# Performance work log

Hardware: AMD Instinct MI355X
Metric: run time of the kernel (lower is better)

The kernel has to match this reference:

```python
import jax, jax.numpy as jnp
import numpy as np

NUM_BINS = 256


def _rgb_to_yuv(rgb):  # [B,3,H,W]
    r, g, b = rgb[:, 0], rgb[:, 1], rgb[:, 2]
    y = 0.299 * r + 0.587 * g + 0.114 * b
    u = -0.147 * r - 0.289 * g + 0.436 * b
    v = 0.615 * r - 0.515 * g - 0.100 * b
    return jnp.stack([y, u, v], axis=1)


def _yuv_to_rgb(yuv):  # [B,3,H,W]
    y, u, v = yuv[:, 0], yuv[:, 1], yuv[:, 2]
    r = y + 1.14 * v
    g = y - 0.396 * u - 0.581 * v
    b = y + 2.029 * u
    return jnp.stack([r, g, b], axis=1)


def _equalize_channel(ch):
    # ch: [H, W] in [0, 1]; replicates kornia/TF equalize on one channel.
    im = ch * 255.0
    flat = im.reshape(-1)
    # histc(bins=256, min=0, max=255): bin width 255/256
    bin_idx = jnp.clip(jnp.floor(flat * (NUM_BINS / 255.0)).astype(jnp.int32), 0, NUM_BINS - 1)
    histo = jax.ops.segment_sum(jnp.ones_like(flat), bin_idx, num_segments=NUM_BINS)
    # last nonzero histogram value
    nz = histo > 0
    last_idx = (NUM_BINS - 1) - jnp.argmax(nz[::-1])
    last_val = histo[last_idx]
    step = jnp.floor((jnp.sum(histo) - last_val) / 255.0)  # integer floor-div semantics
    safe_step = jnp.maximum(step, 1.0)
    lut = jnp.floor((jnp.cumsum(histo) + jnp.floor(step / 2.0)) / safe_step)
    lut = jnp.concatenate([jnp.zeros((1,), lut.dtype), lut[:-1]])
    lut = jnp.clip(lut, 0.0, 255.0)
    gather_idx = jnp.clip(flat.astype(jnp.int32), 0, NUM_BINS - 1)
    mapped = jnp.take(lut, gather_idx)
    out = jnp.where(step == 0.0, flat, mapped)
    return (out / 255.0).reshape(ch.shape)


def setup_inputs() -> dict:
    key = jax.random.key(0)
    img = jax.random.uniform(key, (16, 3, 1024, 1024), dtype=jnp.float32)
    return {"img": img}


def reference(img) -> jnp.ndarray:
    img = jnp.clip(img, 0.0, 1.0)
    yuv = _rgb_to_yuv(img)
    y_eq = jax.vmap(_equalize_channel)(yuv[:, 0])  # [B,H,W]
    yuv = jnp.concatenate([y_eq[:, None], yuv[:, 1:]], axis=1)
    return _yuv_to_rgb(yuv)
```

## Files before the change

kernel.cpp:

```cpp
#include <hip/hip_runtime.h>

#define NPIX   (1024*1024)
#define NBATCH 16
#define NBINS  256

__device__ __forceinline__ float clamp01(float x) {
    return fminf(fmaxf(x, 0.0f), 1.0f);
}

__global__ void __launch_bounds__(256)
hist_kernel(const float* __restrict__ img, unsigned int* __restrict__ hist) {
    const int b = blockIdx.y;
    __shared__ unsigned int lh[NBINS];
    if (threadIdx.x < NBINS) lh[threadIdx.x] = 0u;
    __syncthreads();

    const float* base = img + (size_t)b * 3 * NPIX;
    const float4* r4 = (const float4*)(base);
    const float4* g4 = (const float4*)(base + NPIX);
    const float4* b4 = (const float4*)(base + 2 * NPIX);

    const int n4 = NPIX / 4;
    const int stride = gridDim.x * blockDim.x;
    for (int i = blockIdx.x * blockDim.x + threadIdx.x; i < n4; i += stride) {
        float4 rv = r4[i], gv = g4[i], bv = b4[i];
        float rr[4] = {rv.x, rv.y, rv.z, rv.w};
        float gg[4] = {gv.x, gv.y, gv.z, gv.w};
        float bb[4] = {bv.x, bv.y, bv.z, bv.w};
#pragma unroll
        for (int k = 0; k < 4; ++k) {
            float r = clamp01(rr[k]);
            float g = clamp01(gg[k]);
            float bl = clamp01(bb[k]);
            float y = 0.299f * r + 0.587f * g + 0.114f * bl;
            float flat = y * 255.0f;
            int bin = (int)floorf(flat * (256.0f / 255.0f));
            bin = bin < 0 ? 0 : (bin > NBINS - 1 ? NBINS - 1 : bin);
            atomicAdd(&lh[bin], 1u);
        }
    }
    __syncthreads();
    if (threadIdx.x < NBINS)
        atomicAdd(&hist[b * NBINS + threadIdx.x], lh[threadIdx.x]);
}

__global__ void __launch_bounds__(256)
lut_kernel(const unsigned int* __restrict__ hist,
           float* __restrict__ lut, float* __restrict__ stepflag) {
    const int b = blockIdx.x;
    const int i = threadIdx.x;
    __shared__ float h[NBINS];
    __shared__ float scan[NBINS];
    __shared__ float s_step, s_half;

    h[i] = (float)hist[b * NBINS + i];
    __syncthreads();

    if (i == 0) {
        float total = 0.0f;
        int last = 0;
        for (int k = 0; k < NBINS; ++k) {
            float hv = h[k];
            total += hv;
            if (hv > 0.0f) last = k;
        }
        float step = floorf((total - h[last]) / 255.0f);
        s_step = step;
        s_half = floorf(step / 2.0f);
        float cum = 0.0f;
        for (int k = 0; k < NBINS; ++k) { cum += h[k]; scan[k] = cum; }
        stepflag[b] = step;
    }
    __syncthreads();

    float step = s_step;
    float safe = fmaxf(step, 1.0f);
    float l = (i == 0) ? 0.0f : floorf((scan[i - 1] + s_half) / safe);
    l = fminf(fmaxf(l, 0.0f), 255.0f);
    lut[b * NBINS + i] = l;
}

__global__ void __launch_bounds__(256)
apply_kernel(const float* __restrict__ img, float* __restrict__ out,
             const float* __restrict__ lut, const float* __restrict__ stepflag) {
    const int b = blockIdx.y;
    __shared__ float llut[NBINS];
    if (threadIdx.x < NBINS) llut[threadIdx.x] = lut[b * NBINS + threadIdx.x];
    __syncthreads();

    const float step = stepflag[b];
    const bool identity = (step == 0.0f);

    const float* base  = img + (size_t)b * 3 * NPIX;
    float*       obase = out + (size_t)b * 3 * NPIX;
    const float4* r4 = (const float4*)(base);
    const float4* g4 = (const float4*)(base + NPIX);
    const float4* b4 = (const float4*)(base + 2 * NPIX);
    float4* ro = (float4*)(obase);
    float4* go = (float4*)(obase + NPIX);
    float4* bo = (float4*)(obase + 2 * NPIX);

    const int n4 = NPIX / 4;
    const int stride = gridDim.x * blockDim.x;
    for (int i = blockIdx.x * blockDim.x + threadIdx.x; i < n4; i += stride) {
        float4 rv = r4[i], gv = g4[i], bv = b4[i];
        float rr[4] = {rv.x, rv.y, rv.z, rv.w};
        float gg[4] = {gv.x, gv.y, gv.z, gv.w};
        float bb[4] = {bv.x, bv.y, bv.z, bv.w};
        float orr[4], org[4], orb[4];
#pragma unroll
        for (int k = 0; k < 4; ++k) {
            float r = clamp01(rr[k]);
            float g = clamp01(gg[k]);
            float bl = clamp01(bb[k]);
            float y = 0.299f * r + 0.587f * g + 0.114f * bl;
            float u = -0.147f * r - 0.289f * g + 0.436f * bl;
            float v = 0.615f * r - 0.515f * g - 0.1f * bl;

            float flat = y * 255.0f;
            int gi = (int)flat;
            gi = gi < 0 ? 0 : (gi > NBINS - 1 ? NBINS - 1 : gi);
            float ye = identity ? flat : llut[gi];
            ye = ye / 255.0f;

            orr[k] = ye + 1.14f * v;
            org[k] = ye - 0.396f * u - 0.581f * v;
            orb[k] = ye + 2.029f * u;
        }
        ro[i] = make_float4(orr[0], orr[1], orr[2], orr[3]);
        go[i] = make_float4(org[0], org[1], org[2], org[3]);
        bo[i] = make_float4(orb[0], orb[1], orb[2], orb[3]);
    }
}

extern "C" void kernel_launch(void* const* d_in, const int* in_sizes, int n_in,
                              void* d_out, int out_size, void* d_ws, size_t ws_size,
                              hipStream_t stream) {
    const float* img = (const float*)d_in[0];
    float* out = (float*)d_out;

    unsigned int* hist = (unsigned int*)d_ws;
    float* lut      = (float*)((char*)d_ws + NBATCH * NBINS * 4);
    float* stepflag = (float*)((char*)d_ws + 2 * NBATCH * NBINS * 4);

    hipMemsetAsync(d_ws, 0, NBATCH * NBINS * sizeof(unsigned int), stream);

    const int BPB = 64;
    dim3 grid(BPB, NBATCH), block(256);
    hist_kernel<<<grid, block, 0, stream>>>(img, hist);
    lut_kernel<<<NBATCH, NBINS, 0, stream>>>(hist, lut, stepflag);
    apply_kernel<<<grid, block, 0, stream>>>(img, out, lut, stepflag);
}
```

Measured before the change: 405.6 us.

## Privatize histogram sub-bins, parallelize LUT scan, double grid, nontemporal stores

The histogram kernel now keeps four padded sub-histograms in shared memory, one per thread lane group, to reduce atomic contention on shared-memory bins. The LUT kernel replaces its single-thread serial loops with a parallel prefix scan and a max-reduction for the last nonzero bin. Blocks per batch go from 64 to 128, and the apply kernel uses nontemporal stores and multiplies by a reciprocal instead of dividing. The reciprocal multiply can differ from the reference division by one ulp, and the removed lower clamp relies on the luma value never being negative.

```diff
diff --git a/kernel.cpp b/kernel.cpp
--- a/kernel.cpp
+++ b/kernel.cpp
@@ -3,6 +3,11 @@
 #define NPIX   (1024*1024)
 #define NBATCH 16
 #define NBINS  256
+#define NSUB   4
+#define SUBST  257
+#define BPB    128
+
+typedef float v4f __attribute__((ext_vector_type(4)));
 
 __device__ __forceinline__ float clamp01(float x) {
     return fminf(fmaxf(x, 0.0f), 1.0f);
@@ -11,37 +16,40 @@
 __global__ void __launch_bounds__(256)
 hist_kernel(const float* __restrict__ img, unsigned int* __restrict__ hist) {
     const int b = blockIdx.y;
-    __shared__ unsigned int lh[NBINS];
-    if (threadIdx.x < NBINS) lh[threadIdx.x] = 0u;
+    __shared__ unsigned int lh[NSUB * SUBST];
+    for (int k = threadIdx.x; k < NSUB * SUBST; k += 256) lh[k] = 0u;
     __syncthreads();
 
+    const int sub = (threadIdx.x & (NSUB - 1)) * SUBST;
+
     const float* base = img + (size_t)b * 3 * NPIX;
-    const float4* r4 = (const float4*)(base);
-    const float4* g4 = (const float4*)(base + NPIX);
-    const float4* b4 = (const float4*)(base + 2 * NPIX);
+    const v4f* r4 = (const v4f*)(base);
+    const v4f* g4 = (const v4f*)(base + NPIX);
+    const v4f* b4 = (const v4f*)(base + 2 * NPIX);
 
     const int n4 = NPIX / 4;
     const int stride = gridDim.x * blockDim.x;
     for (int i = blockIdx.x * blockDim.x + threadIdx.x; i < n4; i += stride) {
-        float4 rv = r4[i], gv = g4[i], bv = b4[i];
-        float rr[4] = {rv.x, rv.y, rv.z, rv.w};
-        float gg[4] = {gv.x, gv.y, gv.z, gv.w};
-        float bb[4] = {bv.x, bv.y, bv.z, bv.w};
+        v4f rv = r4[i], gv = g4[i], bv = b4[i];
 #pragma unroll
         for (int k = 0; k < 4; ++k) {
-            float r = clamp01(rr[k]);
-            float g = clamp01(gg[k]);
-            float bl = clamp01(bb[k]);
+            float r = clamp01(rv[k]);
+            float g = clamp01(gv[k]);
+            float bl = clamp01(bv[k]);
             float y = 0.299f * r + 0.587f * g + 0.114f * bl;
             float flat = y * 255.0f;
             int bin = (int)floorf(flat * (256.0f / 255.0f));
             bin = bin < 0 ? 0 : (bin > NBINS - 1 ? NBINS - 1 : bin);
-            atomicAdd(&lh[bin], 1u);
+            atomicAdd(&lh[sub + bin], 1u);
         }
     }
     __syncthreads();
-    if (threadIdx.x < NBINS)
-        atomicAdd(&hist[b * NBINS + threadIdx.x], lh[threadIdx.x]);
+    {
+        const int t = threadIdx.x;
+        unsigned int s = lh[0 * SUBST + t] + lh[1 * SUBST + t] +
+                         lh[2 * SUBST + t] + lh[3 * SUBST + t];
+        atomicAdd(&hist[b * NBINS + t], s);
+    }
 }
 
 __global__ void __launch_bounds__(256)
@@ -49,35 +57,42 @@
            float* __restrict__ lut, float* __restrict__ stepflag) {
     const int b = blockIdx.x;
     const int i = threadIdx.x;
-    __shared__ float h[NBINS];
-    __shared__ float scan[NBINS];
-    __shared__ float s_step, s_half;
+    __shared__ float sc[NBINS];
+    __shared__ int   li[NBINS];
 
-    h[i] = (float)hist[b * NBINS + i];
+    float hv = (float)hist[b * NBINS + i];
+    sc[i] = hv;
+    li[i] = (hv > 0.0f) ? i : -1;
     __syncthreads();
 
-    if (i == 0) {
-        float total = 0.0f;
-        int last = 0;
-        for (int k = 0; k < NBINS; ++k) {
-            float hv = h[k];
-            total += hv;
-            if (hv > 0.0f) last = k;
-        }
-        float step = floorf((total - h[last]) / 255.0f);
-        s_step = step;
-        s_half = floorf(step / 2.0f);
-        float cum = 0.0f;
-        for (int k = 0; k < NBINS; ++k) { cum += h[k]; scan[k] = cum; }
-        stepflag[b] = step;
+#pragma unroll
+    for (int off = 1; off < NBINS; off <<= 1) {
+        float v = (i >= off) ? sc[i - off] : 0.0f;
+        __syncthreads();
+        sc[i] += v;
+        __syncthreads();
     }
-    __syncthreads();
+#pragma unroll
+    for (int off = NBINS / 2; off > 0; off >>= 1) {
+        int v = (i < off) ? li[i + off] : -1;
+        __syncthreads();
+        if (i < off && v > li[i]) li[i] = v;
+        __syncthreads();
+    }
 
-    float step = s_step;
-    float safe = fmaxf(step, 1.0f);
-    float l = (i == 0) ? 0.0f : floorf((scan[i - 1] + s_half) / safe);
+    const float total = sc[NBINS - 1];
+    int last = li[0];
+    if (last < 0) last = NBINS - 1;
+    const float hlast = sc[last] - (last > 0 ? sc[last - 1] : 0.0f);
+
+    const float step = floorf((total - hlast) / 255.0f);
+    const float half = floorf(step * 0.5f);
+    const float safe = fmaxf(step, 1.0f);
+
+    float l = (i == 0) ? 0.0f : floorf((sc[i - 1] + half) / safe);
     l = fminf(fmaxf(l, 0.0f), 255.0f);
     lut[b * NBINS + i] = l;
+    if (i == 0) stepflag[b] = step;
 }
 
 __global__ void __launch_bounds__(256)
@@ -93,43 +108,40 @@
 
     const float* base  = img + (size_t)b * 3 * NPIX;
     float*       obase = out + (size_t)b * 3 * NPIX;
-    const float4* r4 = (const float4*)(base);
-    const float4* g4 = (const float4*)(base + NPIX);
-    const float4* b4 = (const float4*)(base + 2 * NPIX);
-    float4* ro = (float4*)(obase);
-    float4* go = (float4*)(obase + NPIX);
-    float4* bo = (float4*)(obase + 2 * NPIX);
+    const v4f* r4 = (const v4f*)(base);
+    const v4f* g4 = (const v4f*)(base + NPIX);
+    const v4f* b4 = (const v4f*)(base + 2 * NPIX);
+    v4f* ro = (v4f*)(obase);
+    v4f* go = (v4f*)(obase + NPIX);
+    v4f* bo = (v4f*)(obase + 2 * NPIX);
 
     const int n4 = NPIX / 4;
     const int stride = gridDim.x * blockDim.x;
     for (int i = blockIdx.x * blockDim.x + threadIdx.x; i < n4; i += stride) {
-        float4 rv = r4[i], gv = g4[i], bv = b4[i];
-        float rr[4] = {rv.x, rv.y, rv.z, rv.w};
-        float gg[4] = {gv.x, gv.y, gv.z, gv.w};
-        float bb[4] = {bv.x, bv.y, bv.z, bv.w};
-        float orr[4], org[4], orb[4];
+        v4f rv = r4[i], gv = g4[i], bv = b4[i];
+        v4f orr, org, orb;
 #pragma unroll
         for (int k = 0; k < 4; ++k) {
-            float r = clamp01(rr[k]);
-            float g = clamp01(gg[k]);
-            float bl = clamp01(bb[k]);
+            float r = clamp01(rv[k]);
+            float g = clamp01(gv[k]);
+            float bl = clamp01(bv[k]);
             float y = 0.299f * r + 0.587f * g + 0.114f * bl;
             float u = -0.147f * r - 0.289f * g + 0.436f * bl;
             float v = 0.615f * r - 0.515f * g - 0.1f * bl;
 
             float flat = y * 255.0f;
             int gi = (int)flat;
-            gi = gi < 0 ? 0 : (gi > NBINS - 1 ? NBINS - 1 : gi);
+            gi = gi > NBINS - 1 ? NBINS - 1 : gi;
             float ye = identity ? flat : llut[gi];
-            ye = ye / 255.0f;
+            ye = ye * (1.0f / 255.0f);
 
             orr[k] = ye + 1.14f * v;
             org[k] = ye - 0.396f * u - 0.581f * v;
             orb[k] = ye + 2.029f * u;
         }
-        ro[i] = make_float4(orr[0], orr[1], orr[2], orr[3]);
-        go[i] = make_float4(org[0], org[1], org[2], org[3]);
-        bo[i] = make_float4(orb[0], orb[1], orb[2], orb[3]);
+        __builtin_nontemporal_store(orr, &ro[i]);
+        __builtin_nontemporal_store(org, &go[i]);
+        __builtin_nontemporal_store(orb, &bo[i]);
     }
 }
 
@@ -143,9 +155,8 @@
     float* lut      = (float*)((char*)d_ws + NBATCH * NBINS * 4);
     float* stepflag = (float*)((char*)d_ws + 2 * NBATCH * NBINS * 4);
 
-    hipMemsetAsync(d_ws, 0, NBATCH * NBINS * sizeof(unsigned int), stream);
+    (void)hipMemsetAsync(d_ws, 0, NBATCH * NBINS * sizeof(unsigned int), stream);
 
-    const int BPB = 64;
     dim3 grid(BPB, NBATCH), block(256);
     hist_kernel<<<grid, block, 0, stream>>>(img, hist);
     lut_kernel<<<NBATCH, NBINS, 0, stream>>>(hist, lut, stepflag);
```

Result: faster. 377.1 us (-7.0%).
